# Optimization experiments

Measured on AMD Instinct MI355X. Metric: run time of the kernel, lower is better.

## Reference

```python
import jax, jax.numpy as jnp
from jax import lax
import numpy as np

C = 64
K = 3  # kernel_size
PAD = K // 2


def setup_inputs() -> dict:
    key = jax.random.key(0)
    k1, k2, k3, k4, k5 = jax.random.split(key, 5)
    B, N, H, W = 2, 16, 96, 96
    x = jax.random.normal(k1, (B, C, N, H, W), dtype=jnp.float32)
    # offset conv: Conv2d(C, 2K, kernel=(1,K)) -> 1D conv weight (2K, C, K)
    w_off = jax.random.normal(k2, (2 * K, C, K), dtype=jnp.float32) * 0.05
    b_off = jax.random.normal(k3, (2 * K,), dtype=jnp.float32) * 0.05
    # deform conv: DeformConv2d(C, C, kernel=(1,K)) -> weight (C, C, K)
    w_def = jax.random.normal(k4, (C, C, K), dtype=jnp.float32) * (1.0 / np.sqrt(C * K))
    b_def = jax.random.normal(k5, (C,), dtype=jnp.float32) * 0.01
    return {"x": x, "w_off": w_off, "b_off": b_off, "w_def": w_def, "b_def": b_def}


def _deform_fuse(x, w_off, b_off, w_def, b_def):
    B, Cc, N, H, W = x.shape
    M = B * H * W
    # (B,C,N,H,W) -> (B,H,W,C,N) -> (M, C, N); the 'width' axis is the focus axis N
    xm = jnp.transpose(x, (0, 3, 4, 1, 2)).reshape(M, Cc, N)

    # offset-predicting 1D conv over N, padding K//2 (same)
    offsets = lax.conv_general_dilated(
        xm, w_off, window_strides=(1,), padding=[(PAD, PAD)],
        dimension_numbers=("NCH", "OIH", "NCH"),
    ) + b_off[None, :, None]  # (M, 2K, N)
    # torchvision ordering: per kernel tap j, channel 2j = dy, 2j+1 = dx
    off_y = offsets[:, 0::2]  # (M, K, N)
    off_x = offsets[:, 1::2]  # (M, K, N)

    # base sampling positions along the (width=N) axis: n - pad + j
    pos = (jnp.arange(N, dtype=x.dtype)[None, :] - PAD
           + jnp.arange(K, dtype=x.dtype)[:, None])  # (K, N)
    px = pos[None] + off_x                            # (M, K, N)
    x0 = jnp.floor(px)
    fx = px - x0                                      # fractional part
    x0i = x0.astype(jnp.int32)
    x1i = x0i + 1
    v0 = ((x0i >= 0) & (x0i < N)).astype(x.dtype)
    v1 = ((x1i >= 0) & (x1i < N)).astype(x.dtype)
    c0 = jnp.clip(x0i, 0, N - 1)
    c1 = jnp.clip(x1i, 0, N - 1)

    # gather along N per row: (C,N) indexed by (K,N) -> (C,K,N)
    gather = jax.vmap(lambda xr, idx: xr[:, idx])
    g0 = gather(xm, c0) * (v0 * (1.0 - fx))[:, None]   # (M, C, K, N)
    g1 = gather(xm, c1) * (v1 * fx)[:, None]
    # height dim is size 1: bilinear weight along y collapses to relu(1-|dy|)
    wy = jnp.maximum(jnp.array(0.0, x.dtype), 1.0 - jnp.abs(off_y))[:, None]  # (M,1,K,N)
    val = (g0 + g1) * wy                               # (M, C, K, N)

    out = jnp.einsum("ock,mckn->mon", w_def, val) + b_def[None, :, None]  # (M, C, N)
    out = out.reshape(B, H, W, Cc, N)
    return jnp.transpose(out, (0, 3, 4, 1, 2))         # (B, C, N, H, W)


def reference(x, w_off, b_off, w_def, b_def):
    return _deform_fuse(x, w_off, b_off, w_def, b_def)
```

## Files before the change

### kernel.cpp

```cpp
#include <hip/hip_runtime.h>
#include <stdint.h>


typedef __attribute__((ext_vector_type(8))) short short8;
typedef __attribute__((ext_vector_type(4))) float f32x4;

#define XT_OFF   0
#define XG_OFF   18432
#define OFFS_OFF 18432
#define LDS_BYTES 34816

__device__ __forceinline__ short f2bf(float f) {
  union { float f; uint32_t u; } v; v.f = f;
  uint32_t r = (v.u + 0x7FFFu + ((v.u >> 16) & 1u)) >> 16;
  return (short)r;
}
__device__ __forceinline__ float bf2f(short s) {
  union { uint32_t u; float f; } v; v.u = ((uint32_t)(uint16_t)s) << 16; return v.f;
}

__global__ __launch_bounds__(256) void prep_kernel(
    const float* __restrict__ w_off, const float* __restrict__ w_def, short8* __restrict__ ws)
{
  int gid = blockIdx.x * 256 + threadIdx.x;
  if (gid < 1536) {
    int mt = gid / 384, ks = (gid % 384) >> 6, ll = gid & 63;
    int m = mt * 16 + (ll & 15), rgq = ll >> 4;
    short8 v;
    #pragma unroll
    for (int jj = 0; jj < 8; ++jj) {
      int kk = ks * 32 + rgq * 8 + jj;
      int c = kk & 63, k3 = kk >> 6;
      v[jj] = f2bf(w_def[m * 192 + c * 3 + k3]);
    }
    ws[gid] = v;
  } else if (gid < 1920) {
    int q = gid - 1536;
    int ks = q >> 6, ll = q & 63;
    int m = ll & 15, rgq = ll >> 4;
    short8 v;
    #pragma unroll
    for (int jj = 0; jj < 8; ++jj) {
      int kk = ks * 32 + rgq * 8 + jj;
      int c = kk & 63, k3 = kk >> 6;
      v[jj] = (m < 6) ? f2bf(w_off[m * 192 + c * 3 + k3]) : (short)0;
    }
    ws[gid] = v;
  }
}

__global__ __launch_bounds__(256, 4) void deform_main(
    const float* __restrict__ x, const float* __restrict__ b_off,
    const float* __restrict__ b_def, const short8* __restrict__ wfr,
    float* __restrict__ out)
{
  extern __shared__ char smem[];
  uint16_t* xst = (uint16_t*)(smem + XG_OFF);
  float* offs   = (float*)(smem + OFFS_OFF);
  float* stg    = (float*)(smem + XT_OFF);

  const int t = threadIdx.x, wv = t >> 6, l = t & 63, col = l & 15, rg = l >> 4;
  const int p = blockIdx.x;
  const int tn = (p & ~15) | ((p & 7) << 1) | ((p >> 3) & 1);
  const int wt = tn % 12, bh = tn / 12;
  const int h = bh % 96, b = bh / 96, w0 = wt * 8;
  const float* xb = x + (size_t)b * 9437184 + h * 96 + w0;

  #pragma unroll
  for (int i = 0; i < 8; ++i) {
    int r = (t >> 1) + i * 128, half = t & 1;
    float4 v = *(const float4*)(xb + (size_t)r * 9216 + half * 4);
    uint32_t p0 = (uint32_t)(uint16_t)f2bf(v.x) | ((uint32_t)(uint16_t)f2bf(v.y) << 16);
    uint32_t p1 = (uint32_t)(uint16_t)f2bf(v.z) | ((uint32_t)(uint16_t)f2bf(v.w) << 16);
    uint2 pk; pk.x = p0; pk.y = p1;
    *(uint2*)(xst + r * 8 + half * 4) = pk;
  }
  __syncthreads();

  #pragma unroll
  for (int i = 0; i < 4; ++i) {
    int item = t + 256 * i;
    int pos = item & 127, cg = item >> 7;
    short8 v;
    #pragma unroll
    for (int jj = 0; jj < 8; ++jj) v[jj] = (short)xst[(cg * 8 + jj) * 128 + pos];
    *(short8*)(smem + XT_OFF + pos * 144 + cg * 16) = v;
  }
  __syncthreads();

  {
    f32x4 cacc[2] = {{0.f,0.f,0.f,0.f},{0.f,0.f,0.f,0.f}};
    const short8 zero = {0,0,0,0,0,0,0,0};
    #pragma unroll
    for (int ks = 0; ks < 6; ++ks) {
      short8 av = wfr[1536 + ks * 64 + l];
      int k3 = ks >> 1;
      #pragma unroll
      for (int nt2 = 0; nt2 < 2; ++nt2) {
        int pos = (wv * 2 + nt2) * 16 + col;
        int n = pos >> 3, w = pos & 7;
        int row = n + k3 - 1;
        bool valid = (row >= 0) && (row < 16);
        int rcl = min(max(row, 0), 15);
        short8 bv = *(short8*)(smem + XT_OFF + (rcl * 8 + w) * 144 + rg * 16 + (ks & 1) * 64);
        bv = valid ? bv : zero;
        cacc[nt2] = __builtin_amdgcn_mfma_f32_16x16x32_bf16(av, bv, cacc[nt2], 0, 0, 0);
      }
    }
    #pragma unroll
    for (int nt2 = 0; nt2 < 2; ++nt2) {
      int pos = (wv * 2 + nt2) * 16 + col;
      #pragma unroll
      for (int r = 0; r < 4; ++r) {
        int rowo = rg * 4 + r;
        if (rowo < 6) offs[rowo * 128 + pos] = cacc[nt2][r];
      }
    }
  }

  float a0v[3][2], a1v[3][2]; int rb[3][2];
  #pragma unroll
  for (int k = 0; k < 3; ++k) {
    #pragma unroll
    for (int nt2 = 0; nt2 < 2; ++nt2) {
      int pos = (wv * 2 + nt2) * 16 + col;
      int n = pos >> 3, w = pos & 7;
      float oy = offs[(2 * k) * 128 + pos] + b_off[2 * k];
      float ox = offs[(2 * k + 1) * 128 + pos] + b_off[2 * k + 1];
      float px = (float)(n - 1 + k) + ox;
      float x0f = floorf(px);
      float fx = px - x0f;
      int x0 = (int)x0f;
      float wy = fmaxf(0.f, 1.f - fabsf(oy));
      float wt1v = fx * wy;
      float wt0v = wy - wt1v;
      float a0, a1; int r0;
      if (x0 >= 0 && x0 < 15)  { r0 = x0; a0 = wt0v; a1 = wt1v; }
      else if (x0 == 15)       { r0 = 14; a0 = 0.f;  a1 = wt0v; }
      else if (x0 == -1)       { r0 = 0;  a0 = wt1v; a1 = 0.f;  }
      else                     { r0 = 0;  a0 = 0.f;  a1 = 0.f;  }
      a0v[k][nt2] = a0; a1v[k][nt2] = a1;
      rb[k][nt2] = (r0 * 8 + w) * 144;
    }
  }

  f32x4 acc[4][2];
  #pragma unroll
  for (int mt = 0; mt < 4; ++mt) {
    float4 bd = *(const float4*)(b_def + mt * 16 + rg * 4);
    #pragma unroll
    for (int nt2 = 0; nt2 < 2; ++nt2) {
      acc[mt][nt2][0] = bd.x; acc[mt][nt2][1] = bd.y;
      acc[mt][nt2][2] = bd.z; acc[mt][nt2][3] = bd.w;
    }
  }
  #pragma unroll
  for (int k3 = 0; k3 < 3; ++k3) {
    #pragma unroll
    for (int ks2 = 0; ks2 < 2; ++ks2) {
      int ks = k3 * 2 + ks2;
      short8 A[4];
      #pragma unroll
      for (int mt = 0; mt < 4; ++mt) A[mt] = wfr[(mt * 6 + ks) * 64 + l];
      #pragma unroll
      for (int nt2 = 0; nt2 < 2; ++nt2) {
        const char* base = smem + XT_OFF + rb[k3][nt2] + rg * 16 + ks2 * 64;
        short8 x0 = *(const short8*)base;
        short8 x1 = *(const short8*)(base + 1152);
        short8 bv;
        #pragma unroll
        for (int jj = 0; jj < 8; ++jj)
          bv[jj] = f2bf(a0v[k3][nt2] * bf2f(x0[jj]) + a1v[k3][nt2] * bf2f(x1[jj]));
        #pragma unroll
        for (int mt = 0; mt < 4; ++mt)
          acc[mt][nt2] = __builtin_amdgcn_mfma_f32_16x16x32_bf16(A[mt], bv, acc[mt][nt2], 0, 0, 0);
      }
    }
  }
  __syncthreads();

  #pragma unroll
  for (int mt = 0; mt < 4; ++mt) {
    #pragma unroll
    for (int nt2 = 0; nt2 < 2; ++nt2) {
      int pos = (wv * 2 + nt2) * 16 + col;
      #pragma unroll
      for (int r = 0; r < 4; ++r) {
        int o = mt * 16 + rg * 4 + r;
        stg[o * 132 + pos] = acc[mt][nt2][r];
      }
    }
  }
  __syncthreads();
  float* ob = out + (size_t)b * 9437184 + h * 96 + w0;
  #pragma unroll
  for (int i = 0; i < 8; ++i) {
    int s2 = t + 256 * i;
    int q = s2 >> 1, half = s2 & 1;
    int o = q >> 4, n = q & 15;
    float4 v = *(float4*)(stg + o * 132 + n * 8 + half * 4);
    *(float4*)(ob + (size_t)(o * 16 + n) * 9216 + half * 4) = v;
  }
}

extern "C" void kernel_launch(void* const* d_in, const int* in_sizes, int n_in,
                              void* d_out, int out_size, void* d_ws, size_t ws_size,
                              hipStream_t stream) {
  (void)in_sizes; (void)n_in; (void)ws_size; (void)out_size;
  const float* x     = (const float*)d_in[0];
  const float* w_off = (const float*)d_in[1];
  const float* b_off = (const float*)d_in[2];
  const float* w_def = (const float*)d_in[3];
  const float* b_def = (const float*)d_in[4];
  float* out = (float*)d_out;
  short8* wfr = (short8*)d_ws;

  (void)hipFuncSetAttribute((const void*)deform_main,
                            hipFuncAttributeMaxDynamicSharedMemorySize, LDS_BYTES);
  prep_kernel<<<dim3(8), dim3(256), 0, stream>>>(w_off, w_def, wfr);
  deform_main<<<dim3(2304), dim3(256), LDS_BYTES, stream>>>(x, b_off, b_def, wfr, out);
}
```

Measured before the change: 182.0 us.

## Persist blocks over three tiles, prefetching next tile's input during compute

The grid shrinks from 2304 to 768 blocks, and each block now handles three tiles. The global loads for the next tile are issued into registers before the current tile's offset conv and deform GEMM, so load latency overlaps compute. The output staging through LDS is removed in favour of direct scattered float stores. The bf16 packing and interpolation now use v_cvt_pk_bf16 and packed float2 math. Occupancy drops to 3 blocks per CU because of the register cost of holding prefetched data. The direct stores are less coalesced than the old staged float4 writes.

```diff
diff --git a/kernel.cpp b/kernel.cpp
--- a/kernel.cpp
+++ b/kernel.cpp
@@ -4,19 +4,30 @@
 
 typedef __attribute__((ext_vector_type(8))) short short8;
 typedef __attribute__((ext_vector_type(4))) float f32x4;
+typedef __attribute__((ext_vector_type(2))) float f32x2;
+typedef __attribute__((ext_vector_type(4))) unsigned int u32x4;
 
 #define XT_OFF   0
 #define XG_OFF   18432
-#define OFFS_OFF 18432
-#define LDS_BYTES 34816
+#define OFFS_OFF 34816
+#define LDS_BYTES 37888
 
 __device__ __forceinline__ short f2bf(float f) {
   union { float f; uint32_t u; } v; v.f = f;
   uint32_t r = (v.u + 0x7FFFu + ((v.u >> 16) & 1u)) >> 16;
   return (short)r;
 }
-__device__ __forceinline__ float bf2f(short s) {
-  union { uint32_t u; float f; } v; v.u = ((uint32_t)(uint16_t)s) << 16; return v.f;
+__device__ __forceinline__ float asf(uint32_t u) {
+  union { uint32_t u; float f; } v; v.u = u; return v.f;
+}
+__device__ __forceinline__ uint32_t cvt_pk_bf16(float lo, float hi) {
+  uint32_t d;
+  asm("v_cvt_pk_bf16_f32 %0, %1, %2" : "=v"(d) : "v"(lo), "v"(hi));
+  return d;
+}
+__device__ __forceinline__ void wg_barrier() {
+  asm volatile("s_waitcnt lgkmcnt(0)" ::: "memory");
+  __builtin_amdgcn_s_barrier();
 }
 
 __global__ __launch_bounds__(256) void prep_kernel(
@@ -49,7 +60,7 @@
   }
 }
 
-__global__ __launch_bounds__(256, 4) void deform_main(
+__global__ __launch_bounds__(256, 3) void deform_main(
     const float* __restrict__ x, const float* __restrict__ b_off,
     const float* __restrict__ b_def, const short8* __restrict__ wfr,
     float* __restrict__ out)
@@ -57,149 +68,183 @@
   extern __shared__ char smem[];
   uint16_t* xst = (uint16_t*)(smem + XG_OFF);
   float* offs   = (float*)(smem + OFFS_OFF);
-  float* stg    = (float*)(smem + XT_OFF);
 
   const int t = threadIdx.x, wv = t >> 6, l = t & 63, col = l & 15, rg = l >> 4;
   const int p = blockIdx.x;
-  const int tn = (p & ~15) | ((p & 7) << 1) | ((p >> 3) & 1);
-  const int wt = tn % 12, bh = tn / 12;
-  const int h = bh % 96, b = bh / 96, w0 = wt * 8;
-  const float* xb = x + (size_t)b * 9437184 + h * 96 + w0;
+  const int f = (p & ~15) | ((p & 7) << 1) | ((p >> 3) & 1);
+
+  const float* xb = nullptr; float* ob = nullptr;
+  auto set_tile = [&](int jj) {
+    int tn = jj * 768 + f;
+    int wt = tn % 12, bh = tn / 12;
+    int h = bh % 96, b = bh / 96;
+    size_t base = (size_t)b * 9437184 + (size_t)h * 96 + (size_t)(wt * 8);
+    xb = x + base; ob = out + base;
+  };
+
+  float4 v[8];
+  auto load8 = [&]() {
+    #pragma unroll
+    for (int i = 0; i < 8; ++i) {
+      int r = (t >> 1) + i * 128, half = t & 1;
+      v[i] = *(const float4*)(xb + (size_t)r * 9216 + half * 4);
+    }
+  };
+  auto stage_write = [&]() {
+    #pragma unroll
+    for (int i = 0; i < 8; ++i) {
+      int r = (t >> 1) + i * 128, half = t & 1;
+      uint2 pk;
+      pk.x = cvt_pk_bf16(v[i].x, v[i].y);
+      pk.y = cvt_pk_bf16(v[i].z, v[i].w);
+      *(uint2*)(xst + r * 8 + half * 4) = pk;
+    }
+  };
+  auto transpose_ = [&]() {
+    #pragma unroll
+    for (int i = 0; i < 4; ++i) {
+      int item = t + 256 * i;
+      int pos = item & 127, cg = item >> 7;
+      short8 vv;
+      #pragma unroll
+      for (int jj = 0; jj < 8; ++jj) vv[jj] = (short)xst[(cg * 8 + jj) * 128 + pos];
+      *(short8*)(smem + XT_OFF + pos * 144 + cg * 16) = vv;
+    }
+  };
+
+  set_tile(0);
+  load8();
+  stage_write();
+  wg_barrier();
+  transpose_();
+  wg_barrier();
 
   #pragma unroll
-  for (int i = 0; i < 8; ++i) {
-    int r = (t >> 1) + i * 128, half = t & 1;
-    float4 v = *(const float4*)(xb + (size_t)r * 9216 + half * 4);
-    uint32_t p0 = (uint32_t)(uint16_t)f2bf(v.x) | ((uint32_t)(uint16_t)f2bf(v.y) << 16);
-    uint32_t p1 = (uint32_t)(uint16_t)f2bf(v.z) | ((uint32_t)(uint16_t)f2bf(v.w) << 16);
-    uint2 pk; pk.x = p0; pk.y = p1;
-    *(uint2*)(xst + r * 8 + half * 4) = pk;
-  }
-  __syncthreads();
-
-  #pragma unroll
-  for (int i = 0; i < 4; ++i) {
-    int item = t + 256 * i;
-    int pos = item & 127, cg = item >> 7;
-    short8 v;
-    #pragma unroll
-    for (int jj = 0; jj < 8; ++jj) v[jj] = (short)xst[(cg * 8 + jj) * 128 + pos];
-    *(short8*)(smem + XT_OFF + pos * 144 + cg * 16) = v;
-  }
-  __syncthreads();
-
-  {
-    f32x4 cacc[2] = {{0.f,0.f,0.f,0.f},{0.f,0.f,0.f,0.f}};
-    const short8 zero = {0,0,0,0,0,0,0,0};
-    #pragma unroll
-    for (int ks = 0; ks < 6; ++ks) {
-      short8 av = wfr[1536 + ks * 64 + l];
-      int k3 = ks >> 1;
+  for (int j = 0; j < 3; ++j) {
+    float* ob_cur = ob;
+    if (j < 2) {
+      set_tile(j + 1);
+      load8();
+      __builtin_amdgcn_sched_barrier(0);
+    }
+
+    {
+      f32x4 cacc[2] = {{0.f,0.f,0.f,0.f},{0.f,0.f,0.f,0.f}};
+      const short8 zero = {0,0,0,0,0,0,0,0};
+      #pragma unroll
+      for (int ks = 0; ks < 6; ++ks) {
+        short8 av = wfr[1536 + ks * 64 + l];
+        int k3 = ks >> 1;
+        #pragma unroll
+        for (int nt2 = 0; nt2 < 2; ++nt2) {
+          int pos = (wv * 2 + nt2) * 16 + col;
+          int n = pos >> 3, w = pos & 7;
+          int row = n + k3 - 1;
+          bool valid = (row >= 0) && (row < 16);
+          int rcl = min(max(row, 0), 15);
+          short8 bv = *(short8*)(smem + XT_OFF + (rcl * 8 + w) * 144 + rg * 16 + (ks & 1) * 64);
+          bv = valid ? bv : zero;
+          cacc[nt2] = __builtin_amdgcn_mfma_f32_16x16x32_bf16(av, bv, cacc[nt2], 0, 0, 0);
+        }
+      }
+      #pragma unroll
+      for (int nt2 = 0; nt2 < 2; ++nt2) {
+        int pos = (wv * 2 + nt2) * 16 + col;
+        #pragma unroll
+        for (int r = 0; r < 4; ++r) {
+          int rowo = rg * 4 + r;
+          if (rowo < 6) offs[rowo * 128 + pos] = cacc[nt2][r];
+        }
+      }
+    }
+
+    float a0v[3][2], a1v[3][2]; int rb[3][2];
+    #pragma unroll
+    for (int k = 0; k < 3; ++k) {
       #pragma unroll
       for (int nt2 = 0; nt2 < 2; ++nt2) {
         int pos = (wv * 2 + nt2) * 16 + col;
         int n = pos >> 3, w = pos & 7;
-        int row = n + k3 - 1;
-        bool valid = (row >= 0) && (row < 16);
-        int rcl = min(max(row, 0), 15);
-        short8 bv = *(short8*)(smem + XT_OFF + (rcl * 8 + w) * 144 + rg * 16 + (ks & 1) * 64);
-        bv = valid ? bv : zero;
-        cacc[nt2] = __builtin_amdgcn_mfma_f32_16x16x32_bf16(av, bv, cacc[nt2], 0, 0, 0);
-      }
-    }
-    #pragma unroll
-    for (int nt2 = 0; nt2 < 2; ++nt2) {
-      int pos = (wv * 2 + nt2) * 16 + col;
-      #pragma unroll
-      for (int r = 0; r < 4; ++r) {
-        int rowo = rg * 4 + r;
-        if (rowo < 6) offs[rowo * 128 + pos] = cacc[nt2][r];
-      }
-    }
-  }
-
-  float a0v[3][2], a1v[3][2]; int rb[3][2];
-  #pragma unroll
-  for (int k = 0; k < 3; ++k) {
-    #pragma unroll
-    for (int nt2 = 0; nt2 < 2; ++nt2) {
-      int pos = (wv * 2 + nt2) * 16 + col;
-      int n = pos >> 3, w = pos & 7;
-      float oy = offs[(2 * k) * 128 + pos] + b_off[2 * k];
-      float ox = offs[(2 * k + 1) * 128 + pos] + b_off[2 * k + 1];
-      float px = (float)(n - 1 + k) + ox;
-      float x0f = floorf(px);
-      float fx = px - x0f;
-      int x0 = (int)x0f;
-      float wy = fmaxf(0.f, 1.f - fabsf(oy));
-      float wt1v = fx * wy;
-      float wt0v = wy - wt1v;
-      float a0, a1; int r0;
-      if (x0 >= 0 && x0 < 15)  { r0 = x0; a0 = wt0v; a1 = wt1v; }
-      else if (x0 == 15)       { r0 = 14; a0 = 0.f;  a1 = wt0v; }
-      else if (x0 == -1)       { r0 = 0;  a0 = wt1v; a1 = 0.f;  }
-      else                     { r0 = 0;  a0 = 0.f;  a1 = 0.f;  }
-      a0v[k][nt2] = a0; a1v[k][nt2] = a1;
-      rb[k][nt2] = (r0 * 8 + w) * 144;
-    }
-  }
-
-  f32x4 acc[4][2];
-  #pragma unroll
-  for (int mt = 0; mt < 4; ++mt) {
-    float4 bd = *(const float4*)(b_def + mt * 16 + rg * 4);
-    #pragma unroll
-    for (int nt2 = 0; nt2 < 2; ++nt2) {
-      acc[mt][nt2][0] = bd.x; acc[mt][nt2][1] = bd.y;
-      acc[mt][nt2][2] = bd.z; acc[mt][nt2][3] = bd.w;
-    }
-  }
-  #pragma unroll
-  for (int k3 = 0; k3 < 3; ++k3) {
-    #pragma unroll
-    for (int ks2 = 0; ks2 < 2; ++ks2) {
-      int ks = k3 * 2 + ks2;
-      short8 A[4];
-      #pragma unroll
-      for (int mt = 0; mt < 4; ++mt) A[mt] = wfr[(mt * 6 + ks) * 64 + l];
-      #pragma unroll
-      for (int nt2 = 0; nt2 < 2; ++nt2) {
-        const char* base = smem + XT_OFF + rb[k3][nt2] + rg * 16 + ks2 * 64;
-        short8 x0 = *(const short8*)base;
-        short8 x1 = *(const short8*)(base + 1152);
-        short8 bv;
-        #pragma unroll
-        for (int jj = 0; jj < 8; ++jj)
-          bv[jj] = f2bf(a0v[k3][nt2] * bf2f(x0[jj]) + a1v[k3][nt2] * bf2f(x1[jj]));
-        #pragma unroll
-        for (int mt = 0; mt < 4; ++mt)
-          acc[mt][nt2] = __builtin_amdgcn_mfma_f32_16x16x32_bf16(A[mt], bv, acc[mt][nt2], 0, 0, 0);
-      }
-    }
-  }
-  __syncthreads();
-
-  #pragma unroll
-  for (int mt = 0; mt < 4; ++mt) {
-    #pragma unroll
-    for (int nt2 = 0; nt2 < 2; ++nt2) {
-      int pos = (wv * 2 + nt2) * 16 + col;
-      #pragma unroll
-      for (int r = 0; r < 4; ++r) {
-        int o = mt * 16 + rg * 4 + r;
-        stg[o * 132 + pos] = acc[mt][nt2][r];
-      }
-    }
-  }
-  __syncthreads();
-  float* ob = out + (size_t)b * 9437184 + h * 96 + w0;
-  #pragma unroll
-  for (int i = 0; i < 8; ++i) {
-    int s2 = t + 256 * i;
-    int q = s2 >> 1, half = s2 & 1;
-    int o = q >> 4, n = q & 15;
-    float4 v = *(float4*)(stg + o * 132 + n * 8 + half * 4);
-    *(float4*)(ob + (size_t)(o * 16 + n) * 9216 + half * 4) = v;
+        float oy = offs[(2 * k) * 128 + pos] + b_off[2 * k];
+        float ox = offs[(2 * k + 1) * 128 + pos] + b_off[2 * k + 1];
+        float px = (float)(n - 1 + k) + ox;
+        float x0f = floorf(px);
+        float fx = px - x0f;
+        int x0 = (int)x0f;
+        float wy = fmaxf(0.f, 1.f - fabsf(oy));
+        float wt1v = fx * wy;
+        float wt0v = wy - wt1v;
+        float a0, a1; int r0;
+        if (x0 >= 0 && x0 < 15)  { r0 = x0; a0 = wt0v; a1 = wt1v; }
+        else if (x0 == 15)       { r0 = 14; a0 = 0.f;  a1 = wt0v; }
+        else if (x0 == -1)       { r0 = 0;  a0 = wt1v; a1 = 0.f;  }
+        else                     { r0 = 0;  a0 = 0.f;  a1 = 0.f;  }
+        a0v[k][nt2] = a0; a1v[k][nt2] = a1;
+        rb[k][nt2] = (r0 * 8 + w) * 144;
+      }
+    }
+
+    f32x4 acc[4][2];
+    #pragma unroll
+    for (int mt = 0; mt < 4; ++mt) {
+      float4 bd = *(const float4*)(b_def + mt * 16 + rg * 4);
+      #pragma unroll
+      for (int nt2 = 0; nt2 < 2; ++nt2) {
+        acc[mt][nt2][0] = bd.x; acc[mt][nt2][1] = bd.y;
+        acc[mt][nt2][2] = bd.z; acc[mt][nt2][3] = bd.w;
+      }
+    }
+    #pragma unroll
+    for (int k3 = 0; k3 < 3; ++k3) {
+      #pragma unroll
+      for (int ks2 = 0; ks2 < 2; ++ks2) {
+        int ks = k3 * 2 + ks2;
+        short8 A[4];
+        #pragma unroll
+        for (int mt = 0; mt < 4; ++mt) A[mt] = wfr[(mt * 6 + ks) * 64 + l];
+        #pragma unroll
+        for (int nt2 = 0; nt2 < 2; ++nt2) {
+          const char* base = smem + XT_OFF + rb[k3][nt2] + rg * 16 + ks2 * 64;
+          u32x4 x0 = *(const u32x4*)base;
+          u32x4 x1 = *(const u32x4*)(base + 1152);
+          f32x2 A0 = {a0v[k3][nt2], a0v[k3][nt2]};
+          f32x2 A1 = {a1v[k3][nt2], a1v[k3][nt2]};
+          union { uint32_t w[4]; short8 s; } bu;
+          #pragma unroll
+          for (int q = 0; q < 4; ++q) {
+            uint32_t u0 = x0[q], u1 = x1[q];
+            f32x2 X0 = { asf(u0 << 16), asf(u0 & 0xffff0000u) };
+            f32x2 X1 = { asf(u1 << 16), asf(u1 & 0xffff0000u) };
+            f32x2 R = A0 * X0 + A1 * X1;
+            bu.w[q] = cvt_pk_bf16(R.x, R.y);
+          }
+          short8 bv = bu.s;
+          #pragma unroll
+          for (int mt = 0; mt < 4; ++mt)
+            acc[mt][nt2] = __builtin_amdgcn_mfma_f32_16x16x32_bf16(A[mt], bv, acc[mt][nt2], 0, 0, 0);
+        }
+      }
+    }
+
+    #pragma unroll
+    for (int mt = 0; mt < 4; ++mt) {
+      #pragma unroll
+      for (int nt2 = 0; nt2 < 2; ++nt2) {
+        int pos = (wv * 2 + nt2) * 16 + col;
+        int n = pos >> 3, w = pos & 7;
+        float* o0 = ob_cur + (size_t)((mt * 16 + rg * 4) * 16 + n) * 9216 + w;
+        #pragma unroll
+        for (int r = 0; r < 4; ++r)
+          o0[(size_t)r * 147456] = acc[mt][nt2][r];
+      }
+    }
+
+    if (j < 2) {
+      stage_write();
+      wg_barrier();
+      transpose_();
+      wg_barrier();
+    }
   }
 }
 
@@ -218,5 +263,5 @@
   (void)hipFuncSetAttribute((const void*)deform_main,
                             hipFuncAttributeMaxDynamicSharedMemorySize, LDS_BYTES);
   prep_kernel<<<dim3(8), dim3(256), 0, stream>>>(w_off, w_def, wfr);
-  deform_main<<<dim3(2304), dim3(256), LDS_BYTES, stream>>>(x, b_off, b_def, wfr, out);
-}
+  deform_main<<<dim3(768), dim3(256), LDS_BYTES, stream>>>(x, b_off, b_def, wfr, out);
+}
```

Measured after the change: 221.2 us. +21.5%, slower.

## Widen block tile to 16 columns and store outputs directly from registers

Applied to the files above, without the earlier changes.

Each block now covers 16 w positions with 512 threads, giving 8 waves where there were 4, and LDS is doubled to hold the larger tile. The epilogue drops the LDS staging pass and its barriers: each lane writes its accumulator values straight to global memory as 64-byte row segments. bf16 conversion now uses the hardware v_cvt_pk_bf16_f32 instruction, and the interpolation uses packed float2 math. Risks are lower occupancy from the larger LDS footprint, less coalesced output stores, and removal of the block-index swizzle.

```diff
diff --git a/kernel.cpp b/kernel.cpp
--- a/kernel.cpp
+++ b/kernel.cpp
@@ -4,19 +4,26 @@
 
 typedef __attribute__((ext_vector_type(8))) short short8;
 typedef __attribute__((ext_vector_type(4))) float f32x4;
+typedef __attribute__((ext_vector_type(2))) float f32x2;
+typedef __attribute__((ext_vector_type(4))) unsigned int u32x4;
 
 #define XT_OFF   0
-#define XG_OFF   18432
-#define OFFS_OFF 18432
-#define LDS_BYTES 34816
+#define XG_OFF   36864
+#define OFFS_OFF 36864
+#define LDS_BYTES 69632
 
 __device__ __forceinline__ short f2bf(float f) {
   union { float f; uint32_t u; } v; v.f = f;
   uint32_t r = (v.u + 0x7FFFu + ((v.u >> 16) & 1u)) >> 16;
   return (short)r;
 }
-__device__ __forceinline__ float bf2f(short s) {
-  union { uint32_t u; float f; } v; v.u = ((uint32_t)(uint16_t)s) << 16; return v.f;
+__device__ __forceinline__ float asf(uint32_t u) {
+  union { uint32_t u; float f; } v; v.u = u; return v.f;
+}
+__device__ __forceinline__ uint32_t cvt_pk_bf16(float lo, float hi) {
+  uint32_t d;
+  asm("v_cvt_pk_bf16_f32 %0, %1, %2" : "=v"(d) : "v"(lo), "v"(hi));
+  return d;
 }
 
 __global__ __launch_bounds__(256) void prep_kernel(
@@ -49,7 +56,7 @@
   }
 }
 
-__global__ __launch_bounds__(256, 4) void deform_main(
+__global__ __launch_bounds__(512, 4) void deform_main(
     const float* __restrict__ x, const float* __restrict__ b_off,
     const float* __restrict__ b_def, const short8* __restrict__ wfr,
     float* __restrict__ out)
@@ -57,34 +64,32 @@
   extern __shared__ char smem[];
   uint16_t* xst = (uint16_t*)(smem + XG_OFF);
   float* offs   = (float*)(smem + OFFS_OFF);
-  float* stg    = (float*)(smem + XT_OFF);
 
   const int t = threadIdx.x, wv = t >> 6, l = t & 63, col = l & 15, rg = l >> 4;
-  const int p = blockIdx.x;
-  const int tn = (p & ~15) | ((p & 7) << 1) | ((p >> 3) & 1);
-  const int wt = tn % 12, bh = tn / 12;
-  const int h = bh % 96, b = bh / 96, w0 = wt * 8;
+  const int tn = blockIdx.x;
+  const int wt = tn % 6, bh = tn / 6;
+  const int h = bh % 96, b = bh / 96, w0 = wt * 16;
   const float* xb = x + (size_t)b * 9437184 + h * 96 + w0;
 
   #pragma unroll
   for (int i = 0; i < 8; ++i) {
-    int r = (t >> 1) + i * 128, half = t & 1;
-    float4 v = *(const float4*)(xb + (size_t)r * 9216 + half * 4);
-    uint32_t p0 = (uint32_t)(uint16_t)f2bf(v.x) | ((uint32_t)(uint16_t)f2bf(v.y) << 16);
-    uint32_t p1 = (uint32_t)(uint16_t)f2bf(v.z) | ((uint32_t)(uint16_t)f2bf(v.w) << 16);
-    uint2 pk; pk.x = p0; pk.y = p1;
-    *(uint2*)(xst + r * 8 + half * 4) = pk;
+    int r = (t >> 2) + i * 128, quad = t & 3;
+    float4 v = *(const float4*)(xb + (size_t)r * 9216 + quad * 4);
+    uint2 pk;
+    pk.x = cvt_pk_bf16(v.x, v.y);
+    pk.y = cvt_pk_bf16(v.z, v.w);
+    *(uint2*)(xst + r * 16 + quad * 4) = pk;
   }
   __syncthreads();
 
   #pragma unroll
   for (int i = 0; i < 4; ++i) {
-    int item = t + 256 * i;
-    int pos = item & 127, cg = item >> 7;
-    short8 v;
-    #pragma unroll
-    for (int jj = 0; jj < 8; ++jj) v[jj] = (short)xst[(cg * 8 + jj) * 128 + pos];
-    *(short8*)(smem + XT_OFF + pos * 144 + cg * 16) = v;
+    int item = t + 512 * i;
+    int pos = item & 255, cg = item >> 8;
+    short8 vv;
+    #pragma unroll
+    for (int jj = 0; jj < 8; ++jj) vv[jj] = (short)xst[(cg * 8 + jj) * 256 + pos];
+    *(short8*)(smem + XT_OFF + pos * 144 + cg * 16) = vv;
   }
   __syncthreads();
 
@@ -97,12 +102,11 @@
       int k3 = ks >> 1;
       #pragma unroll
       for (int nt2 = 0; nt2 < 2; ++nt2) {
-        int pos = (wv * 2 + nt2) * 16 + col;
-        int n = pos >> 3, w = pos & 7;
+        int n = wv * 2 + nt2;
         int row = n + k3 - 1;
         bool valid = (row >= 0) && (row < 16);
         int rcl = min(max(row, 0), 15);
-        short8 bv = *(short8*)(smem + XT_OFF + (rcl * 8 + w) * 144 + rg * 16 + (ks & 1) * 64);
+        short8 bv = *(short8*)(smem + XT_OFF + (rcl * 16 + col) * 144 + rg * 16 + (ks & 1) * 64);
         bv = valid ? bv : zero;
         cacc[nt2] = __builtin_amdgcn_mfma_f32_16x16x32_bf16(av, bv, cacc[nt2], 0, 0, 0);
       }
@@ -113,7 +117,7 @@
       #pragma unroll
       for (int r = 0; r < 4; ++r) {
         int rowo = rg * 4 + r;
-        if (rowo < 6) offs[rowo * 128 + pos] = cacc[nt2][r];
+        if (rowo < 6) offs[rowo * 256 + pos] = cacc[nt2][r];
       }
     }
   }
@@ -123,10 +127,10 @@
   for (int k = 0; k < 3; ++k) {
     #pragma unroll
     for (int nt2 = 0; nt2 < 2; ++nt2) {
-      int pos = (wv * 2 + nt2) * 16 + col;
-      int n = pos >> 3, w = pos & 7;
-      float oy = offs[(2 * k) * 128 + pos] + b_off[2 * k];
-      float ox = offs[(2 * k + 1) * 128 + pos] + b_off[2 * k + 1];
+      int n = wv * 2 + nt2;
+      int pos = n * 16 + col;
+      float oy = offs[(2 * k) * 256 + pos] + b_off[2 * k];
+      float ox = offs[(2 * k + 1) * 256 + pos] + b_off[2 * k + 1];
       float px = (float)(n - 1 + k) + ox;
       float x0f = floorf(px);
       float fx = px - x0f;
@@ -140,7 +144,7 @@
       else if (x0 == -1)       { r0 = 0;  a0 = wt1v; a1 = 0.f;  }
       else                     { r0 = 0;  a0 = 0.f;  a1 = 0.f;  }
       a0v[k][nt2] = a0; a1v[k][nt2] = a1;
-      rb[k][nt2] = (r0 * 8 + w) * 144;
+      rb[k][nt2] = (r0 * 16 + col) * 144;
     }
   }
 
@@ -165,41 +169,38 @@
       #pragma unroll
       for (int nt2 = 0; nt2 < 2; ++nt2) {
         const char* base = smem + XT_OFF + rb[k3][nt2] + rg * 16 + ks2 * 64;
-        short8 x0 = *(const short8*)base;
-        short8 x1 = *(const short8*)(base + 1152);
-        short8 bv;
+        u32x4 x0 = *(const u32x4*)base;
+        u32x4 x1 = *(const u32x4*)(base + 2304);
+        f32x2 A0 = {a0v[k3][nt2], a0v[k3][nt2]};
+        f32x2 A1 = {a1v[k3][nt2], a1v[k3][nt2]};
+        union { uint32_t w[4]; short8 s; } bu;
         #pragma unroll
-        for (int jj = 0; jj < 8; ++jj)
-          bv[jj] = f2bf(a0v[k3][nt2] * bf2f(x0[jj]) + a1v[k3][nt2] * bf2f(x1[jj]));
+        for (int q = 0; q < 4; ++q) {
+          uint32_t u0 = x0[q], u1 = x1[q];
+          f32x2 X0 = { asf(u0 << 16), asf(u0 & 0xffff0000u) };
+          f32x2 X1 = { asf(u1 << 16), asf(u1 & 0xffff0000u) };
+          f32x2 R = A0 * X0 + A1 * X1;
+          bu.w[q] = cvt_pk_bf16(R.x, R.y);
+        }
+        short8 bv = bu.s;
         #pragma unroll
         for (int mt = 0; mt < 4; ++mt)
           acc[mt][nt2] = __builtin_amdgcn_mfma_f32_16x16x32_bf16(A[mt], bv, acc[mt][nt2], 0, 0, 0);
       }
     }
   }
-  __syncthreads();
-
+
+  float* ob = out + (size_t)b * 9437184 + h * 96 + w0;
   #pragma unroll
   for (int mt = 0; mt < 4; ++mt) {
     #pragma unroll
     for (int nt2 = 0; nt2 < 2; ++nt2) {
-      int pos = (wv * 2 + nt2) * 16 + col;
-      #pragma unroll
-      for (int r = 0; r < 4; ++r) {
-        int o = mt * 16 + rg * 4 + r;
-        stg[o * 132 + pos] = acc[mt][nt2][r];
-      }
-    }
-  }
-  __syncthreads();
-  float* ob = out + (size_t)b * 9437184 + h * 96 + w0;
-  #pragma unroll
-  for (int i = 0; i < 8; ++i) {
-    int s2 = t + 256 * i;
-    int q = s2 >> 1, half = s2 & 1;
-    int o = q >> 4, n = q & 15;
-    float4 v = *(float4*)(stg + o * 132 + n * 8 + half * 4);
-    *(float4*)(ob + (size_t)(o * 16 + n) * 9216 + half * 4) = v;
+      int n = wv * 2 + nt2;
+      float* o0 = ob + (size_t)((mt * 16 + rg * 4) * 16 + n) * 9216 + col;
+      #pragma unroll
+      for (int r = 0; r < 4; ++r)
+        o0[(size_t)r * 147456] = acc[mt][nt2][r];
+    }
   }
 }
 
@@ -218,5 +219,5 @@
   (void)hipFuncSetAttribute((const void*)deform_main,
                             hipFuncAttributeMaxDynamicSharedMemorySize, LDS_BYTES);
   prep_kernel<<<dim3(8), dim3(256), 0, stream>>>(w_off, w_def, wfr);
-  deform_main<<<dim3(2304), dim3(256), LDS_BYTES, stream>>>(x, b_off, b_def, wfr, out);
-}
+  deform_main<<<dim3(1152), dim3(512), LDS_BYTES, stream>>>(x, b_off, b_def, wfr, out);
+}
```

Result: faster. 171.1 us (-6.0%).
